# Kernel tuning notes

Hardware: AMD Instinct MI355X
Metric: run time of the kernel (lower is better)

The kernel has to match this reference:

```python
import jax, jax.numpy as jnp
import numpy as np

D_MODEL = 1024
N_HEADS = 16
HEAD_DIM = D_MODEL // N_HEADS
SCALE = float(np.sqrt(HEAD_DIM))
NEG_INF = -1e30


def setup_inputs() -> dict:
    key = jax.random.key(0)
    k1, k2, k3 = jax.random.split(key, 3)
    B, S = 4, 2048
    x = jax.random.normal(k1, (B, S, D_MODEL), dtype=jnp.float32)
    attention_mask = jnp.ones((B, S), dtype=jnp.int32)
    # torch Linear(d, 3d, bias=False): y = x @ W^T; store pre-transposed (d, 3d)
    w_qkv = jax.random.normal(k2, (D_MODEL, 3 * D_MODEL), dtype=jnp.float32) * (1.0 / np.sqrt(D_MODEL))
    w_out = jax.random.normal(k3, (D_MODEL, D_MODEL), dtype=jnp.float32) * (1.0 / np.sqrt(D_MODEL))
    return {"x": x, "attention_mask": attention_mask, "w_qkv": w_qkv, "w_out": w_out}


def reference(x, attention_mask, w_qkv, w_out):
    B, S, _ = x.shape
    qkv = jnp.einsum('bsd,de->bse', x, w_qkv)                     # (B,S,3D)
    qkv = qkv.reshape(B, S, 3, N_HEADS, HEAD_DIM)
    q = qkv[:, :, 0].transpose(0, 2, 1, 3)                        # (B,H,S,hd)
    k = qkv[:, :, 1].transpose(0, 2, 1, 3)
    v = qkv[:, :, 2].transpose(0, 2, 1, 3)

    scores = jnp.einsum('bhqd,bhkd->bhqk', q, k) / SCALE          # (B,H,S,S)
    causal_mask = jnp.triu(jnp.ones((S, S), dtype=bool), k=1)     # True above diag
    scores = jnp.where(causal_mask[None, None], NEG_INF, scores)
    pad_mask = (attention_mask == 0)[:, None, None, :]            # (B,1,1,S)
    scores = jnp.where(pad_mask, NEG_INF, scores)

    attn = jax.nn.softmax(scores, axis=-1)                        # dropout=0 (eval)
    out = jnp.einsum('bhqk,bhkd->bhqd', attn, v)                  # (B,H,S,hd)
    out = out.transpose(0, 2, 1, 3).reshape(B, S, D_MODEL)
    return jnp.einsum('bsd,de->bse', out, w_out)
```

## Files before the change

kernel.cpp:

```cpp
#include <hip/hip_runtime.h>


typedef __attribute__((ext_vector_type(8))) short bf16x8;
typedef __attribute__((ext_vector_type(8))) unsigned short u16x8;
typedef __attribute__((ext_vector_type(4))) unsigned short u16x4;
typedef __attribute__((ext_vector_type(4))) float f32x4;

#define MFMA16 __builtin_amdgcn_mfma_f32_16x16x32_bf16

#define GLDS(gp, lp) __builtin_amdgcn_global_load_lds( \
    (const __attribute__((address_space(1))) unsigned int*)(gp), \
    (__attribute__((address_space(3))) unsigned int*)(lp), 16, 0, 0)

__device__ __forceinline__ unsigned short f2bf(float f) {
    union { float f; unsigned int u; } v; v.f = f;
    unsigned int r = v.u + 0x7fffu + ((v.u >> 16) & 1u);
    return (unsigned short)(r >> 16);
}

__global__ void k_prep(const float* __restrict__ x, unsigned short* __restrict__ xb,
                       const int* __restrict__ mask, unsigned short* __restrict__ mb,
                       const float* __restrict__ wqkv, unsigned short* __restrict__ w1t,
                       const float* __restrict__ wout, unsigned short* __restrict__ w2t) {
    __shared__ float tile[32][33];
    const int bx = blockIdx.x;
    if (bx < 4096) {
        size_t i = ((size_t)bx * 256 + threadIdx.x) * 8;
        float4 f0 = *(const float4*)(x + i);
        float4 f1 = *(const float4*)(x + i + 4);
        u16x8 v;
        v[0] = f2bf(f0.x); v[1] = f2bf(f0.y); v[2] = f2bf(f0.z); v[3] = f2bf(f0.w);
        v[4] = f2bf(f1.x); v[5] = f2bf(f1.y); v[6] = f2bf(f1.z); v[7] = f2bf(f1.w);
        *(u16x8*)(xb + i) = v;
        if (bx < 32) {
            int j = bx * 256 + threadIdx.x;
            mb[j] = mask[j] ? (unsigned short)0x3F80 : (unsigned short)0;
        }
    } else {
        const int b2 = bx - 4096;
        const int cb = b2 & 127, rb = b2 >> 7;
        const float* in = (cb < 96) ? wqkv : wout;
        unsigned short* out = (cb < 96) ? w1t : w2t;
        const int C = (cb < 96) ? 3072 : 1024;
        const int c0 = ((cb < 96) ? cb : cb - 96) * 32;
        const int r0 = rb * 32;
        int tx = threadIdx.x & 31, ty = threadIdx.x >> 5;
        for (int i = ty; i < 32; i += 8)
            tile[i][tx] = in[(size_t)(r0 + i) * C + (c0 + tx)];
        __syncthreads();
        for (int i = ty; i < 32; i += 8)
            out[(size_t)(c0 + i) * 1024 + (r0 + tx)] = f2bf(tile[tx][i]);
    }
}

template <int MODE>
__global__ __launch_bounds__(256) void k_gemm_bt(
    const unsigned short* __restrict__ Ab,
    const unsigned short* __restrict__ Bt,
    float* __restrict__ Cf,
    unsigned short* __restrict__ qb,
    unsigned short* __restrict__ kb,
    unsigned short* __restrict__ vt,
    const int* __restrict__ mask,
    int N, int K)
{
    __shared__ __align__(16) unsigned short la[128 * 64];
    __shared__ __align__(16) unsigned short lb[128 * 64];
    const int t = threadIdx.x;
    const int m0 = blockIdx.y * 128, n0 = blockIdx.x * 128;
    const int w = t >> 6, lane = t & 63;
    const int wm = (w & 1) * 64, wn = (w >> 1) * 64;
    const int lr = lane & 15, lq = lane >> 4;
    const int lr7 = lr & 7;
    const int rowb = lane >> 3;
    const int g8 = (((lane & 7) - rowb) & 7) * 8;

    f32x4 acc[4][4];
    for (int i = 0; i < 4; ++i)
        for (int j = 0; j < 4; ++j)
            acc[i][j] = (f32x4){0.f, 0.f, 0.f, 0.f};

    for (int k0 = 0; k0 < K; k0 += 64) {
        #pragma unroll
        for (int r = 0; r < 4; ++r) {
            const int rg = w * 8 + r * 32;
            GLDS(&Ab[(size_t)(m0 + rg + rowb) * K + k0 + g8], &la[rg * 64]);
            GLDS(&Bt[(size_t)(n0 + rg + rowb) * K + k0 + g8], &lb[rg * 64]);
        }
        __syncthreads();
        #pragma unroll
        for (int ks = 0; ks < 2; ++ks) {
            const int pa = ((ks * 4 + lq + lr7) & 7) * 8;
            bf16x8 af[4], bg[4];
            #pragma unroll
            for (int i = 0; i < 4; ++i) {
                af[i] = *(const bf16x8*)&la[(wm + i * 16 + lr) * 64 + pa];
                bg[i] = *(const bf16x8*)&lb[(wn + i * 16 + lr) * 64 + pa];
            }
            #pragma unroll
            for (int i = 0; i < 4; ++i)
                #pragma unroll
                for (int j = 0; j < 4; ++j)
                    acc[i][j] = MFMA16(af[i], bg[j], acc[i][j], 0, 0, 0);
        }
        __syncthreads();
    }

    const float QSCALE = 0.18033688f;
    if (MODE == 0) {
        for (int i = 0; i < 4; ++i)
            for (int j = 0; j < 4; ++j)
                for (int r = 0; r < 4; ++r) {
                    int row = m0 + wm + i * 16 + lq * 4 + r;
                    int col = n0 + wn + j * 16 + lr;
                    Cf[(size_t)row * N + col] = acc[i][j][r];
                }
    } else {
        const int which = n0 >> 10;
        if (which < 2) {
            unsigned short* dst = which ? kb : qb;
            const float sc = which ? 1.0f : QSCALE;
            for (int i = 0; i < 4; ++i)
                for (int j = 0; j < 4; ++j)
                    for (int r = 0; r < 4; ++r) {
                        int row = m0 + wm + i * 16 + lq * 4 + r;
                        int col = n0 + wn + j * 16 + lr;
                        int h = (col >> 6) & 15, d = col & 63;
                        int b = row >> 11, s = row & 2047;
                        dst[((size_t)(b * 16 + h) * 2048 + s) * 64 + d] = f2bf(acc[i][j][r] * sc);
                    }
        } else {
            for (int i = 0; i < 4; ++i) {
                int s0 = m0 + wm + i * 16 + lq * 4;
                int b = s0 >> 11, s = s0 & 2047;
                int4 m4 = *(const int4*)&mask[b * 2048 + s];
                for (int j = 0; j < 4; ++j) {
                    int col = n0 + wn + j * 16 + lr;
                    int h = (col >> 6) & 15, d = col & 63;
                    u16x4 pv;
                    pv[0] = m4.x ? f2bf(acc[i][j][0]) : (unsigned short)0;
                    pv[1] = m4.y ? f2bf(acc[i][j][1]) : (unsigned short)0;
                    pv[2] = m4.z ? f2bf(acc[i][j][2]) : (unsigned short)0;
                    pv[3] = m4.w ? f2bf(acc[i][j][3]) : (unsigned short)0;
                    *(u16x4*)&vt[((size_t)(b * 16 + h) * 64 + d) * 2048 + s] = pv;
                }
            }
        }
    }
}

__global__ __launch_bounds__(512, 6) void k_attn(
    const unsigned short* __restrict__ qb,
    const unsigned short* __restrict__ kb,
    const unsigned short* __restrict__ vt,
    const unsigned short* __restrict__ maskbg,
    unsigned short* __restrict__ ao)
{
    __shared__ __align__(16) unsigned short kt_lds[2][64 * 64];
    __shared__ __align__(16) unsigned short vt_lds[2][64 * 64];
    __shared__ __align__(16) unsigned short plds[8][16 * 64];

    const int t = threadIdx.x;
    const int w = t >> 6, lane = t & 63;
    const int lr = lane & 15, lq = lane >> 4;
    const int lr7 = lr & 7;
    const int bh = blockIdx.x, b = bh >> 4, h = bh & 15;

    const unsigned short* qp = qb + (size_t)bh * 2048 * 64;
    const unsigned short* kp = kb + (size_t)bh * 2048 * 64;
    const unsigned short* vp = vt + (size_t)bh * 64 * 2048;
    const unsigned short* mbg = maskbg + b * 2048;
    unsigned short* pw = plds[w];

    const int rowb = lane >> 3, c8 = lane & 7;
    const int sc8 = (c8 ^ rowb) * 8;

    auto stage = [&](int c) {
        const int buf = c & 1;
        const int k0 = c * 64;
        const int rg = 8 * w;
        const int row = rg + rowb;
        GLDS(&kp[(size_t)(k0 + row) * 64 + sc8], &kt_lds[buf][rg * 64]);
        GLDS(&vp[(size_t)row * 2048 + k0 + sc8], &vt_lds[buf][rg * 64]);
    };

    const int stripe = 15 - (int)blockIdx.y;
    const int q0w = stripe * 128 + w * 16;

    bf16x8 aq0 = *(const bf16x8*)&qp[(q0w + lr) * 64 + lq * 8];
    bf16x8 aq1 = *(const bf16x8*)&qp[(q0w + lr) * 64 + 32 + lq * 8];

    f32x4 acc[4], lacc;
    lacc = (f32x4){0.f, 0.f, 0.f, 0.f};
    #pragma unroll
    for (int j = 0; j < 4; ++j) acc[j] = (f32x4){0.f, 0.f, 0.f, 0.f};

    const int nch = 2 * (stripe + 1);
    stage(0);
    for (int c = 0; c < nch; ++c) {
        __syncthreads();
        if (c + 1 < nch) stage(c + 1);
        const int k0 = c * 64;
        if (k0 < q0w + 16) {
            const unsigned short* kt = kt_lds[c & 1];
            const unsigned short* vtl = vt_lds[c & 1];
            const bool causal = (k0 + 63 > q0w);
            const int kcol0 = (lq ^ lr7) * 8;
            const int kcol1 = ((4 + lq) ^ lr7) * 8;
            #pragma unroll
            for (int ki = 0; ki < 4; ++ki) {
                bf16x8 kf0 = *(const bf16x8*)&kt[(ki * 16 + lr) * 64 + kcol0];
                bf16x8 kf1 = *(const bf16x8*)&kt[(ki * 16 + lr) * 64 + kcol1];
                f32x4 s = (f32x4){0.f, 0.f, 0.f, 0.f};
                s = MFMA16(kf0, aq0, s, 0, 0, 0);
                s = MFMA16(kf1, aq1, s, 0, 0, 0);
                unsigned int u[4];
                #pragma unroll
                for (int r = 0; r < 4; ++r) {
                    float scv = s[r];
                    if (causal) {
                        int key = k0 + ki * 16 + lq * 4 + r;
                        int qq  = q0w + lr;
                        scv = (key <= qq) ? scv : -3.0e38f;
                    }
                    float p = __builtin_amdgcn_exp2f(scv);
                    union { float f; unsigned int u; } cv; cv.f = p;
                    u[r] = cv.u;
                }
                uint2 pk;
                pk.x = __builtin_amdgcn_perm(u[1], u[0], 0x07060302u);
                pk.y = __builtin_amdgcn_perm(u[3], u[2], 0x07060302u);
                *(uint2*)&pw[lr * 64 + (((ki * 2 + (lq >> 1)) ^ lr7) * 8) + (lq & 1) * 4] = pk;
            }
            #pragma unroll
            for (int kc = 0; kc < 64; kc += 32) {
                bf16x8 pf = *(const bf16x8*)&pw[lr * 64 + ((((kc >> 3) + lq) ^ lr7) * 8)];
                bf16x8 mb = *(const bf16x8*)&mbg[k0 + kc + lq * 8];
                const int vcol = (((kc >> 3) + lq) ^ lr7) * 8;
                #pragma unroll
                for (int j = 0; j < 4; ++j) {
                    bf16x8 vf = *(const bf16x8*)&vtl[(j * 16 + lr) * 64 + vcol];
                    acc[j] = MFMA16(pf, vf, acc[j], 0, 0, 0);
                }
                lacc = MFMA16(pf, mb, lacc, 0, 0, 0);
            }
        }
    }

    #pragma unroll
    for (int r = 0; r < 4; ++r) {
        float inv = 1.0f / fmaxf(lacc[r], 1e-30f);
        int row = q0w + lq * 4 + r;
        #pragma unroll
        for (int j = 0; j < 4; ++j) {
            int d = j * 16 + lr;
            ao[(size_t)(b * 2048 + row) * 1024 + h * 64 + d] = f2bf(acc[j][r] * inv);
        }
    }
}

extern "C" void kernel_launch(void* const* d_in, const int* in_sizes, int n_in,
                              void* d_out, int out_size, void* d_ws, size_t ws_size,
                              hipStream_t stream)
{
    const float* x    = (const float*)d_in[0];
    const int*   mask = (const int*)d_in[1];
    const float* wqkv = (const float*)d_in[2];
    const float* wout = (const float*)d_in[3];
    float* out = (float*)d_out;

    const size_t NEED = ((size_t)8192 * 1024 + (size_t)3072 * 1024 + (size_t)1024 * 1024 +
                         3 * (size_t)64 * 2048 * 64 + (size_t)8192 * 1024 + 8192) * 2;
    if (ws_size < NEED) return;

    char* ws = (char*)d_ws;
    unsigned short* xb  = (unsigned short*)ws; ws += (size_t)8192 * 1024 * 2;
    unsigned short* w1t = (unsigned short*)ws; ws += (size_t)3072 * 1024 * 2;
    unsigned short* w2t = (unsigned short*)ws; ws += (size_t)1024 * 1024 * 2;
    unsigned short* qb  = (unsigned short*)ws; ws += (size_t)64 * 2048 * 64 * 2;
    unsigned short* kb  = (unsigned short*)ws; ws += (size_t)64 * 2048 * 64 * 2;
    unsigned short* vt  = (unsigned short*)ws; ws += (size_t)64 * 64 * 2048 * 2;
    unsigned short* ao  = (unsigned short*)ws; ws += (size_t)8192 * 1024 * 2;
    unsigned short* mbg = (unsigned short*)ws; ws += (size_t)8192 * 2;

    k_prep<<<dim3(8192), 256, 0, stream>>>(x, xb, mask, mbg, wqkv, w1t, wout, w2t);
    k_gemm_bt<1><<<dim3(24, 64), 256, 0, stream>>>(xb, w1t, nullptr, qb, kb, vt, mask, 3072, 1024);
    k_attn<<<dim3(64, 16), 512, 0, stream>>>(qb, kb, vt, mbg, ao);
    k_gemm_bt<0><<<dim3(8, 64), 256, 0, stream>>>(ao, w2t, out, nullptr, nullptr, nullptr, nullptr, 1024, 1024);
}
```

Baseline: 244.4 us.

## Keep attention P in registers via shuffles, add setprio, remap GEMM blocks across XCDs

The attention kernel no longer stages the softmax probability tile through per-wave LDS. It passes packed bf16 pairs between lanes with __shfl to build the MFMA A-operand, which frees LDS, and the launch-bounds occupancy hint is raised from 6 to 8. s_setprio is wrapped around the MFMA groups to favour matrix issue across waves. The GEMM block index is remapped so consecutive tiles land on the same XCD for L2 reuse. The risks are that the shuffles cost more than the LDS round-trip did and that the higher occupancy target causes register spills.

```diff
diff --git a/kernel.cpp b/kernel.cpp
--- a/kernel.cpp
+++ b/kernel.cpp
@@ -53,7 +53,7 @@
     }
 }
 
-template <int MODE>
+template <int MODE, int NBX>
 __global__ __launch_bounds__(256) void k_gemm_bt(
     const unsigned short* __restrict__ Ab,
     const unsigned short* __restrict__ Bt,
@@ -67,7 +67,11 @@
     __shared__ __align__(16) unsigned short la[128 * 64];
     __shared__ __align__(16) unsigned short lb[128 * 64];
     const int t = threadIdx.x;
-    const int m0 = blockIdx.y * 128, n0 = blockIdx.x * 128;
+    const int nwg = NBX * 64;
+    const int cpx = nwg >> 3;
+    const int orig = (int)blockIdx.y * NBX + (int)blockIdx.x;
+    const int rm = (orig & 7) * cpx + (orig >> 3);
+    const int m0 = (rm / NBX) * 128, n0 = (rm % NBX) * 128;
     const int w = t >> 6, lane = t & 63;
     const int wm = (w & 1) * 64, wn = (w >> 1) * 64;
     const int lr = lane & 15, lq = lane >> 4;
@@ -149,7 +153,7 @@
     }
 }
 
-__global__ __launch_bounds__(512, 6) void k_attn(
+__global__ __launch_bounds__(512, 8) void k_attn(
     const unsigned short* __restrict__ qb,
     const unsigned short* __restrict__ kb,
     const unsigned short* __restrict__ vt,
@@ -158,7 +162,6 @@
 {
     __shared__ __align__(16) unsigned short kt_lds[2][64 * 64];
     __shared__ __align__(16) unsigned short vt_lds[2][64 * 64];
-    __shared__ __align__(16) unsigned short plds[8][16 * 64];
 
     const int t = threadIdx.x;
     const int w = t >> 6, lane = t & 63;
@@ -170,7 +173,6 @@
     const unsigned short* kp = kb + (size_t)bh * 2048 * 64;
     const unsigned short* vp = vt + (size_t)bh * 64 * 2048;
     const unsigned short* mbg = maskbg + b * 2048;
-    unsigned short* pw = plds[w];
 
     const int rowb = lane >> 3, c8 = lane & 7;
     const int sc8 = (c8 ^ rowb) * 8;
@@ -207,13 +209,16 @@
             const bool causal = (k0 + 63 > q0w);
             const int kcol0 = (lq ^ lr7) * 8;
             const int kcol1 = ((4 + lq) ^ lr7) * 8;
+            uint2 pk4[4];
             #pragma unroll
             for (int ki = 0; ki < 4; ++ki) {
                 bf16x8 kf0 = *(const bf16x8*)&kt[(ki * 16 + lr) * 64 + kcol0];
                 bf16x8 kf1 = *(const bf16x8*)&kt[(ki * 16 + lr) * 64 + kcol1];
                 f32x4 s = (f32x4){0.f, 0.f, 0.f, 0.f};
+                __builtin_amdgcn_s_setprio(1);
                 s = MFMA16(kf0, aq0, s, 0, 0, 0);
                 s = MFMA16(kf1, aq1, s, 0, 0, 0);
+                __builtin_amdgcn_s_setprio(0);
                 unsigned int u[4];
                 #pragma unroll
                 for (int r = 0; r < 4; ++r) {
@@ -227,22 +232,40 @@
                     union { float f; unsigned int u; } cv; cv.f = p;
                     u[r] = cv.u;
                 }
-                uint2 pk;
-                pk.x = __builtin_amdgcn_perm(u[1], u[0], 0x07060302u);
-                pk.y = __builtin_amdgcn_perm(u[3], u[2], 0x07060302u);
-                *(uint2*)&pw[lr * 64 + (((ki * 2 + (lq >> 1)) ^ lr7) * 8) + (lq & 1) * 4] = pk;
+                pk4[ki].x = __builtin_amdgcn_perm(u[1], u[0], 0x07060302u);
+                pk4[ki].y = __builtin_amdgcn_perm(u[3], u[2], 0x07060302u);
             }
             #pragma unroll
             for (int kc = 0; kc < 64; kc += 32) {
-                bf16x8 pf = *(const bf16x8*)&pw[lr * 64 + ((((kc >> 3) + lq) ^ lr7) * 8)];
+                const int kA = kc >> 4;
+                const int srcA = lr + (lq & 1) * 32;
+                const int srcB = srcA + 16;
+                int r0ax = __shfl((int)pk4[kA].x,     srcA);
+                int r0ay = __shfl((int)pk4[kA].y,     srcA);
+                int r0bx = __shfl((int)pk4[kA].x,     srcB);
+                int r0by = __shfl((int)pk4[kA].y,     srcB);
+                int r1ax = __shfl((int)pk4[kA + 1].x, srcA);
+                int r1ay = __shfl((int)pk4[kA + 1].y, srcA);
+                int r1bx = __shfl((int)pk4[kA + 1].x, srcB);
+                int r1by = __shfl((int)pk4[kA + 1].y, srcB);
+                const bool hi = (lq & 2) != 0;
+                int4 pfi;
+                pfi.x = hi ? r1ax : r0ax;
+                pfi.y = hi ? r1ay : r0ay;
+                pfi.z = hi ? r1bx : r0bx;
+                pfi.w = hi ? r1by : r0by;
+                union { int4 i; bf16x8 v; } cvt; cvt.i = pfi;
+                bf16x8 pf = cvt.v;
                 bf16x8 mb = *(const bf16x8*)&mbg[k0 + kc + lq * 8];
                 const int vcol = (((kc >> 3) + lq) ^ lr7) * 8;
+                __builtin_amdgcn_s_setprio(1);
                 #pragma unroll
                 for (int j = 0; j < 4; ++j) {
                     bf16x8 vf = *(const bf16x8*)&vtl[(j * 16 + lr) * 64 + vcol];
                     acc[j] = MFMA16(pf, vf, acc[j], 0, 0, 0);
                 }
                 lacc = MFMA16(pf, mb, lacc, 0, 0, 0);
+                __builtin_amdgcn_s_setprio(0);
             }
         }
     }
@@ -284,7 +307,7 @@
     unsigned short* mbg = (unsigned short*)ws; ws += (size_t)8192 * 2;
 
     k_prep<<<dim3(8192), 256, 0, stream>>>(x, xb, mask, mbg, wqkv, w1t, wout, w2t);
-    k_gemm_bt<1><<<dim3(24, 64), 256, 0, stream>>>(xb, w1t, nullptr, qb, kb, vt, mask, 3072, 1024);
+    k_gemm_bt<1, 24><<<dim3(24, 64), 256, 0, stream>>>(xb, w1t, nullptr, qb, kb, vt, mask, 3072, 1024);
     k_attn<<<dim3(64, 16), 512, 0, stream>>>(qb, kb, vt, mbg, ao);
-    k_gemm_bt<0><<<dim3(8, 64), 256, 0, stream>>>(ao, w2t, out, nullptr, nullptr, nullptr, nullptr, 1024, 1024);
-}
+    k_gemm_bt<0, 8><<<dim3(8, 64), 256, 0, stream>>>(ao, w2t, out, nullptr, nullptr, nullptr, nullptr, 1024, 1024);
+}
```

Measured after the change: 256.2 us. 1.05x slower.
